# Kernel tuning notes

Measured on AMD Instinct MI355X. Metric: run time of the kernel, lower is better.

Reference implementation:

```python
import jax, jax.numpy as jnp
import numpy as np

B, L, D, H = 2, 4096, 1024, 4
DV = D // H
NP = 5
MIN_PROB = 0.01
CHUNK = 32
RIN = D + H * NP * 4 + H * (NP * (NP - 1)) // 2  # 1144
RH = 2 * RIN


def dwconv_causal(x, w):
    # x: (B, L, C); w: (C, K) depthwise causal FIR
    K = w.shape[-1]
    xp = jnp.pad(x, ((0, 0), (K - 1, 0), (0, 0))).transpose(0, 2, 1)  # (B,C,L+K-1)
    y = jax.lax.conv_general_dilated(
        xp, w[:, None, :], window_strides=(1,), padding='VALID',
        feature_group_count=w.shape[0],
        dimension_numbers=('NCH', 'OIH', 'NCH'))
    return y.transpose(0, 2, 1)  # (B,L,C)


def l2norm(x):
    return x * jax.lax.rsqrt(jnp.sum(x * x, -1, keepdims=True) + 1e-12)


def delta_rule_chunkwise(q, k, v, beta, chunk=CHUNK):
    # q,k: (b,h,L,dk)  v: (b,h,L,dv)  beta: (b,h,L); L divisible by chunk
    b, h, Lq, dk = q.shape
    dv = v.shape[-1]
    n = Lq // chunk
    q = l2norm(q); k = l2norm(k)
    v = v * beta[..., None]
    kb = k * beta[..., None]
    r = lambda x: x.reshape(b, h, n, chunk, -1)
    q, k, v, kb = r(q), r(k), r(v), r(kb)
    tri = jnp.triu(jnp.ones((chunk, chunk), bool), 0)
    attn = jnp.where(tri, 0.0, -(kb @ jnp.swapaxes(k, -1, -2)))
    for i in range(1, chunk):  # in-chunk triangular-inverse recurrence
        upd = jnp.einsum('...k,...ki->...i', attn[..., i, :], attn[..., :, :i])
        attn = attn.at[..., i, :i].add(upd)
    attn = attn + jnp.eye(chunk, dtype=attn.dtype)
    u = attn @ v
    w = attn @ kb
    strict = jnp.triu(jnp.ones((chunk, chunk), bool), 1)

    def step(S, inp):
        qi, ki, ui, wi = inp
        la = jnp.where(strict, 0.0, qi @ jnp.swapaxes(ki, -1, -2))
        u_i = ui - wi @ S
        o_i = qi @ S + la @ u_i
        return S + jnp.swapaxes(ki, -1, -2) @ u_i, o_i

    mv = lambda x: jnp.moveaxis(x, 2, 0)
    S0 = jnp.zeros((b, h, dk, dv), q.dtype)
    S, o = jax.lax.scan(step, S0, (mv(q), mv(k), mv(u), mv(w)))
    return jnp.moveaxis(o, 0, 2).reshape(b, h, Lq, dv), S


def setup_inputs() -> dict:
    key = jax.random.key(0)
    ks = jax.random.split(key, 20)
    f = lambda k, shape, s=0.02: jax.random.normal(k, shape, jnp.float32) * s
    # FIR filters: identity tap (last) + small noise, matching learned-from-delta init
    def fir(k, ksz):
        w = np.zeros((D, ksz), np.float32)
        w[:, -1] = 1.0
        return jnp.asarray(w) + f(k, (D, ksz), 0.02)
    b2 = np.zeros((H, NP), np.float32)
    b2[:, -1] = 0.5
    b2[:, -2] = 0.5
    return {
        'hidden_states': jax.random.normal(ks[0], (B, L, D), jnp.float32),
        'Wq': f(ks[1], (D, D)), 'Wk': f(ks[2], (D, D)), 'Wv': f(ks[3], (D, D)),
        'wq_conv': f(ks[4], (D, 4), 0.2), 'wk_conv': f(ks[5], (D, 4), 0.2),
        'wv_conv': f(ks[6], (D, 4), 0.2),
        'Wb': f(ks[7], (H, D)),
        'fir_s_w': fir(ks[8], 3), 'fir_m_w': fir(ks[9], 7),
        'fir_l_w': fir(ks[10], 25), 'fir_id_w': fir(ks[11], 1),
        'W1': f(ks[12], (RH, RIN)), 'b1': jnp.zeros((RH,), jnp.float32),
        'W2': f(ks[13], (H * NP, RH)), 'b2': jnp.asarray(b2.reshape(-1)),
        'norm_w': jnp.ones((DV,), jnp.float32),
        'Wo': f(ks[14], (D, D)),
    }


def reference(hidden_states, Wq, Wk, Wv, wq_conv, wk_conv, wv_conv, Wb,
              fir_s_w, fir_m_w, fir_l_w, fir_id_w, W1, b1, W2, b2, norm_w, Wo):
    silu = jax.nn.silu
    q = silu(dwconv_causal(hidden_states @ Wq.T, wq_conv))
    k = silu(dwconv_causal(hidden_states @ Wk.T, wk_conv))
    v = silu(dwconv_causal(hidden_states @ Wv.T, wv_conv))
    beta = jax.nn.sigmoid(hidden_states @ Wb.T)  # (B,L,H)
    q4 = q.reshape(B, L, H, -1).transpose(0, 2, 1, 3)
    k4 = k.reshape(B, L, H, -1).transpose(0, 2, 1, 3)
    v4 = v.reshape(B, L, H, -1).transpose(0, 2, 1, 3)
    delta_out, _ = delta_rule_chunkwise(q4, k4, v4, beta.transpose(0, 2, 1))
    delta_out = delta_out.transpose(0, 2, 1, 3)  # (B,L,H,DV)
    fir = lambda w: dwconv_causal(v, w).reshape(B, L, H, DV)
    branches = [fir(fir_s_w), fir(fir_m_w), fir(fir_l_w), delta_out, fir(fir_id_w)]
    feats = []
    for x in branches:
        sm = jax.nn.softmax(x, -1)
        feats += [x.mean(-1), jnp.var(x, -1, ddof=1), jnp.max(x, -1),
                  -(sm * jnp.log(sm + 1e-8)).sum(-1)]
    cross = []
    for i in range(NP):
        for j in range(i + 1, NP):
            xi, xj = branches[i], branches[j]
            den = jnp.sqrt(jnp.sum(xi * xi, -1)) * jnp.sqrt(jnp.sum(xj * xj, -1)) + 1e-8
            cross.append(jnp.sum(xi * xj, -1) / den)
    router_in = jnp.concatenate([hidden_states] + feats + cross, axis=-1)  # (B,L,RIN)
    hrt = jax.nn.gelu(router_in @ W1.T + b1, approximate=False)
    logits = (hrt @ W2.T + b2).reshape(B, L, H, NP)
    p = jax.nn.softmax(logits, -1)
    p = p * (1.0 - NP * MIN_PROB) + MIN_PROB  # probability floor
    out = jnp.einsum('blhp,pblhd->blhd', p, jnp.stack(branches))
    out = out * jax.lax.rsqrt(jnp.mean(out * out, -1, keepdims=True) + 1e-5) * norm_w
    return out.reshape(B, L, H * DV) @ Wo.T
```

## Files before the change

### kernel.cpp

```cpp
#include <hip/hip_runtime.h>
#include <stdint.h>

typedef unsigned short u16t;
typedef u16t us4 __attribute__((ext_vector_type(4)));
typedef u16t us8 __attribute__((ext_vector_type(8)));
typedef __bf16 bf8v __attribute__((ext_vector_type(8)));
typedef float f4 __attribute__((ext_vector_type(4)));

#define MFMA(a, b, c) __builtin_amdgcn_mfma_f32_16x16x32_bf16((a), (b), (c), 0, 0, 0)

__device__ __forceinline__ float bf2f(u16t u) {
  union { unsigned int i; float f; } c; c.i = ((unsigned int)u) << 16; return c.f;
}
__device__ __forceinline__ u16t f2bf(float f) {
  union { float f; unsigned int i; } c; c.f = f;
  return (u16t)((c.i + 0x7FFFu + ((c.i >> 16) & 1u)) >> 16);
}
__device__ __forceinline__ float wsum(float v) {
#pragma unroll
  for (int o = 32; o > 0; o >>= 1) v += __shfl_xor(v, o);
  return v;
}
__device__ __forceinline__ float wmax(float v) {
#pragma unroll
  for (int o = 32; o > 0; o >>= 1) v = fmaxf(v, __shfl_xor(v, o));
  return v;
}

template <bool AF32, bool BF32, bool CF32>
__global__ __launch_bounds__(256) void gemm_bt(const void* __restrict__ Av,
    const void* __restrict__ Btv, void* __restrict__ Cv,
    int M, int N, int K, int lda, int ldb, int ldc) {
  __shared__ u16t As[128][40];
  __shared__ u16t Bs[128][40];
  const int tid = threadIdx.x;
  const int m0 = blockIdx.y * 128, n0 = blockIdx.x * 128;
  const int wv = tid >> 6, l = tid & 63;
  const int wr = wv >> 1, wc = wv & 1;
  const int lr = l & 15, kg8 = (l >> 4) * 8, rg4 = (l >> 4) * 4;
  const int row_s = tid >> 1, seg = (tid & 1) * 16;
  const f4 zf = {0.f, 0.f, 0.f, 0.f};
  f4 acc[4][4];
#pragma unroll
  for (int i = 0; i < 4; ++i)
#pragma unroll
    for (int j = 0; j < 4; ++j) acc[i][j] = zf;

  for (int kt = 0; kt < K; kt += 32) {
    us8 a0, a1, b0, b1;
    if (AF32) {
      const float* pa = (const float*)Av + (size_t)(m0 + row_s) * lda + seg + kt;
      f4 fa0 = *(const f4*)(pa), fa1 = *(const f4*)(pa + 4);
      f4 fa2 = *(const f4*)(pa + 8), fa3 = *(const f4*)(pa + 12);
#pragma unroll
      for (int e = 0; e < 4; ++e) {
        a0[e] = f2bf(fa0[e]); a0[e + 4] = f2bf(fa1[e]);
        a1[e] = f2bf(fa2[e]); a1[e + 4] = f2bf(fa3[e]);
      }
    } else {
      const u16t* pa = (const u16t*)Av + (size_t)(m0 + row_s) * lda + seg + kt;
      a0 = *(const us8*)(pa); a1 = *(const us8*)(pa + 8);
    }
    if (BF32) {
      const float* pb = (const float*)Btv + (size_t)(n0 + row_s) * ldb + seg + kt;
      f4 fb0 = *(const f4*)(pb), fb1 = *(const f4*)(pb + 4);
      f4 fb2 = *(const f4*)(pb + 8), fb3 = *(const f4*)(pb + 12);
#pragma unroll
      for (int e = 0; e < 4; ++e) {
        b0[e] = f2bf(fb0[e]); b0[e + 4] = f2bf(fb1[e]);
        b1[e] = f2bf(fb2[e]); b1[e + 4] = f2bf(fb3[e]);
      }
    } else {
      const u16t* pb = (const u16t*)Btv + (size_t)(n0 + row_s) * ldb + seg + kt;
      b0 = *(const us8*)(pb); b1 = *(const us8*)(pb + 8);
    }
    *(us8*)&As[row_s][seg] = a0;
    *(us8*)&As[row_s][seg + 8] = a1;
    *(us8*)&Bs[row_s][seg] = b0;
    *(us8*)&Bs[row_s][seg + 8] = b1;
    __syncthreads();
    bf8v af[4], bg[4];
#pragma unroll
    for (int f = 0; f < 4; ++f) af[f] = *(const bf8v*)&As[wr * 64 + f * 16 + lr][kg8];
#pragma unroll
    for (int f = 0; f < 4; ++f) bg[f] = *(const bf8v*)&Bs[wc * 64 + f * 16 + lr][kg8];
#pragma unroll
    for (int i = 0; i < 4; ++i)
#pragma unroll
      for (int j = 0; j < 4; ++j) acc[i][j] = MFMA(af[i], bg[j], acc[i][j]);
    __syncthreads();
  }
#pragma unroll
  for (int i = 0; i < 4; ++i) {
    const int rb = m0 + wr * 64 + i * 16 + rg4;
#pragma unroll
    for (int j = 0; j < 4; ++j) {
      const int cb = n0 + wc * 64 + j * 16 + lr;
#pragma unroll
      for (int r = 0; r < 4; ++r) {
        if (CF32)
          ((float*)Cv)[(size_t)(rb + r) * ldc + cb] = acc[i][j][r];
        else
          ((u16t*)Cv)[(size_t)(rb + r) * ldc + cb] = f2bf(acc[i][j][r]);
      }
    }
  }
}

__global__ __launch_bounds__(256) void conv4_silu(
    const u16t* __restrict__ qlin, const u16t* __restrict__ klin, const u16t* __restrict__ vlin,
    const float* __restrict__ wq, const float* __restrict__ wk, const float* __restrict__ wvv,
    u16t* __restrict__ qc, u16t* __restrict__ kc, u16t* __restrict__ vc) {
  const int tid = threadIdx.x;
  const int l0 = blockIdx.x * 64;
  const int b = blockIdx.y >> 2, cb = blockIdx.y & 3;
  const int z = blockIdx.z;
  const u16t* in_ = (z == 0) ? qlin : ((z == 1) ? klin : vlin);
  const float* w_ = (z == 0) ? wq : ((z == 1) ? wk : wvv);
  u16t* out_ = (z == 0) ? qc : ((z == 1) ? kc : vc);
  const int c = cb * 256 + tid;
  __shared__ u16t sm[67][256];
  for (int i = 0; i < 67; ++i) {
    int ls = l0 - 3 + i;
    sm[i][tid] = (ls >= 0) ? in_[((size_t)b * 4096 + ls) * 1024 + c] : (u16t)0;
  }
  __syncthreads();
  f4 w4 = *(const f4*)&w_[c * 4];
  for (int ll = 0; ll < 64; ++ll) {
    float y = bf2f(sm[ll][tid]) * w4[0] + bf2f(sm[ll + 1][tid]) * w4[1] +
              bf2f(sm[ll + 2][tid]) * w4[2] + bf2f(sm[ll + 3][tid]) * w4[3];
    y = y / (1.f + expf(-y));
    out_[((size_t)b * 4096 + l0 + ll) * 1024 + c] = f2bf(y);
  }
}

__global__ __launch_bounds__(256) void beta_kernel(const float* __restrict__ hid,
    const float* __restrict__ Wb, float* __restrict__ beta) {
  const int m = blockIdx.x, tid = threadIdx.x;
  const int h = tid >> 6, l = tid & 63;
  float acc = 0.f;
#pragma unroll
  for (int it = 0; it < 4; ++it) {
    int kk = l * 4 + it * 256;
    f4 hv = *(const f4*)&hid[(size_t)m * 1024 + kk];
    f4 wv4 = *(const f4*)&Wb[(size_t)h * 1024 + kk];
#pragma unroll
    for (int e = 0; e < 4; ++e) acc += hv[e] * wv4[e];
  }
  acc = wsum(acc);
  if (l == 0) beta[m * 4 + h] = 1.f / (1.f + expf(-acc));
}

__global__ __launch_bounds__(256) void prep_kernel(u16t* __restrict__ qc, u16t* __restrict__ kc,
    const u16t* __restrict__ vc, const float* __restrict__ beta,
    u16t* __restrict__ kbeta, u16t* __restrict__ vbeta) {
  const int m = blockIdx.x, tid = threadIdx.x;
  const int h = tid >> 6, l = tid & 63;
  const size_t base = (size_t)m * 1024 + h * 256 + l * 4;
  const float bet = beta[m * 4 + h];
  us4 q4 = *(const us4*)&qc[base];
  float qf[4]; float ss = 0.f;
#pragma unroll
  for (int e = 0; e < 4; ++e) { qf[e] = bf2f(q4[e]); ss += qf[e] * qf[e]; }
  float qsc = rsqrtf(wsum(ss) + 1e-12f);
  us4 qo;
#pragma unroll
  for (int e = 0; e < 4; ++e) qo[e] = f2bf(qf[e] * qsc);
  *(us4*)&qc[base] = qo;
  us4 k4 = *(const us4*)&kc[base];
  float kf[4]; ss = 0.f;
#pragma unroll
  for (int e = 0; e < 4; ++e) { kf[e] = bf2f(k4[e]); ss += kf[e] * kf[e]; }
  float ksc = rsqrtf(wsum(ss) + 1e-12f);
  us4 ko, kbo;
#pragma unroll
  for (int e = 0; e < 4; ++e) {
    float kn = kf[e] * ksc;
    ko[e] = f2bf(kn);
    kbo[e] = f2bf(kn * bet);
  }
  *(us4*)&kc[base] = ko;
  *(us4*)&kbeta[base] = kbo;
  us4 v4 = *(const us4*)&vc[base];
  us4 vo;
#pragma unroll
  for (int e = 0; e < 4; ++e) vo[e] = f2bf(bf2f(v4[e]) * bet);
  *(us4*)&vbeta[base] = vo;
}

__global__ __launch_bounds__(256) void chunk_uw(const u16t* __restrict__ kn,
    const u16t* __restrict__ kbeta, const u16t* __restrict__ vbeta,
    u16t* __restrict__ ug, u16t* __restrict__ wg) {
  const int tid = threadIdx.x;
  const int bh = blockIdx.x >> 7, ci = blockIdx.x & 127;
  const int b = bh >> 2, h = bh & 3;
  const int l0 = ci * 32;
  __shared__ u16t kns[32][264], kbs[32][264], vbs[32][264];
  __shared__ float attn_s[32][33];
  const int sr = tid >> 5, sd8 = (tid & 31) * 8;
  const size_t rowbase = (size_t)b * 4096 * 1024 + (size_t)h * 256;
#pragma unroll
  for (int i = 0; i < 4; ++i) {
    int r = i * 8 + sr;
    size_t g = rowbase + (size_t)(l0 + r) * 1024 + sd8;
    *(us8*)&kns[r][sd8] = *(const us8*)&kn[g];
    *(us8*)&kbs[r][sd8] = *(const us8*)&kbeta[g];
    *(us8*)&vbs[r][sd8] = *(const us8*)&vbeta[g];
  }
  __syncthreads();
  {
    const int i = tid >> 3, j4 = (tid & 7) * 4;
    float d0 = 0.f, d1 = 0.f, d2 = 0.f, d3 = 0.f;
    for (int d8 = 0; d8 < 256; d8 += 8) {
      us8 kb8 = *(const us8*)&kbs[i][d8];
      us8 n0v = *(const us8*)&kns[j4][d8];
      us8 n1v = *(const us8*)&kns[j4 + 1][d8];
      us8 n2v = *(const us8*)&kns[j4 + 2][d8];
      us8 n3v = *(const us8*)&kns[j4 + 3][d8];
#pragma unroll
      for (int e = 0; e < 8; ++e) {
        float kv = bf2f(kb8[e]);
        d0 += kv * bf2f(n0v[e]); d1 += kv * bf2f(n1v[e]);
        d2 += kv * bf2f(n2v[e]); d3 += kv * bf2f(n3v[e]);
      }
    }
    attn_s[i][j4]     = (j4     < i) ? -d0 : 0.f;
    attn_s[i][j4 + 1] = (j4 + 1 < i) ? -d1 : 0.f;
    attn_s[i][j4 + 2] = (j4 + 2 < i) ? -d2 : 0.f;
    attn_s[i][j4 + 3] = (j4 + 3 < i) ? -d3 : 0.f;
  }
  __syncthreads();
  if (tid < 32) {
    const int j = tid;
    for (int i = 1; i < 32; ++i) {
      float aij = attn_s[i][j];
      float upd = 0.f;
#pragma unroll 1
      for (int k = 1; k < 31; ++k) {
        float aik = __shfl(aij, k);
        float akj = (k > j && k < i) ? attn_s[k][j] : 0.f;
        upd += aik * akj;
      }
      if (j < i) attn_s[i][j] = aij + upd;
    }
    attn_s[j][j] = 1.f;
  }
  __syncthreads();
  {
    const int r = tid >> 3, cg = (tid & 7) * 32;
    float ua[32], wa[32];
#pragma unroll
    for (int e = 0; e < 32; ++e) { ua[e] = 0.f; wa[e] = 0.f; }
    for (int j = 0; j < 32; ++j) {
      float a = attn_s[r][j];
#pragma unroll
      for (int e0 = 0; e0 < 32; e0 += 8) {
        us8 v8 = *(const us8*)&vbs[j][cg + e0];
        us8 k8 = *(const us8*)&kbs[j][cg + e0];
#pragma unroll
        for (int e = 0; e < 8; ++e) {
          ua[e0 + e] += a * bf2f(v8[e]);
          wa[e0 + e] += a * bf2f(k8[e]);
        }
      }
    }
    const size_t ob = ((size_t)bh * 4096 + l0 + r) * 256 + cg;
#pragma unroll
    for (int e0 = 0; e0 < 32; e0 += 8) {
      us8 pu, pw;
#pragma unroll
      for (int e = 0; e < 8; ++e) { pu[e] = f2bf(ua[e0 + e]); pw[e] = f2bf(wa[e0 + e]); }
      *(us8*)&ug[ob + e0] = pu;
      *(us8*)&wg[ob + e0] = pw;
    }
  }
}

__global__ __launch_bounds__(256, 1) void delta_scan(const u16t* __restrict__ qn,
    const u16t* __restrict__ kn, const u16t* __restrict__ ug, const u16t* __restrict__ wg,
    u16t* __restrict__ dout) {
  const int blk = blockIdx.x;
  const int bh = blk >> 2, vbidx = blk & 3;
  const int b = bh >> 2, h = bh & 3;
  const int c0 = vbidx * 64;
  const int tid = threadIdx.x;
  const int wv = tid >> 6, l = tid & 63;
  const int lr = l & 15, kg8 = (l >> 4) * 8, rg4 = (l >> 4) * 4;

  __shared__ u16t qs[32][264], ks2[32][264], wss[32][264];
  __shared__ u16t kts[256][40];
  __shared__ u16t sbf[64][264];
  __shared__ u16t las[32][40];
  __shared__ u16t uts[64][40];

  {
    u16t* sp = &sbf[0][0];
    for (int i = tid; i < 64 * 264; i += 256) sp[i] = 0;
  }
  const f4 zf = {0.f, 0.f, 0.f, 0.f};
  f4 sacc[16];
#pragma unroll
  for (int d = 0; d < 16; ++d) sacc[d] = zf;
  __syncthreads();

  const u16t* qb = qn + (size_t)b * 4096 * 1024 + (size_t)h * 256;
  const u16t* knb = kn + (size_t)b * 4096 * 1024 + (size_t)h * 256;
  const u16t* ub = ug + (size_t)bh * 4096 * 256;
  const u16t* wb = wg + (size_t)bh * 4096 * 256;
  const int sr = tid >> 5, sd8 = (tid & 31) * 8;

  us8 pq[4], pk[4], pw[4];
  us4 pu0, pu1;
  {
#pragma unroll
    for (int i = 0; i < 4; ++i) {
      const int r = i * 8 + sr;
      pq[i] = *(const us8*)(qb + (size_t)r * 1024 + sd8);
      pk[i] = *(const us8*)(knb + (size_t)r * 1024 + sd8);
      pw[i] = *(const us8*)(wb + (size_t)r * 256 + sd8);
    }
    pu0 = *(const us4*)(ub + (size_t)lr * 256 + c0 + wv * 16 + rg4);
    pu1 = *(const us4*)(ub + (size_t)(16 + lr) * 256 + c0 + wv * 16 + rg4);
  }

  for (int ci = 0; ci < 128; ++ci) {
    const int l0 = ci * 32;
#pragma unroll
    for (int i = 0; i < 4; ++i) {
      const int r = i * 8 + sr;
      *(us8*)&qs[r][sd8] = pq[i];
      *(us8*)&ks2[r][sd8] = pk[i];
      *(us8*)&wss[r][sd8] = pw[i];
    }
    const us4 u0 = pu0, u1 = pu1;
    __syncthreads();
    if (ci < 127) {
      const int l1 = l0 + 32;
#pragma unroll
      for (int i = 0; i < 4; ++i) {
        const int r = i * 8 + sr;
        pq[i] = *(const us8*)(qb + (size_t)(l1 + r) * 1024 + sd8);
        pk[i] = *(const us8*)(knb + (size_t)(l1 + r) * 1024 + sd8);
        pw[i] = *(const us8*)(wb + (size_t)(l1 + r) * 256 + sd8);
      }
      pu0 = *(const us4*)(ub + (size_t)(l1 + lr) * 256 + c0 + wv * 16 + rg4);
      pu1 = *(const us4*)(ub + (size_t)(l1 + 16 + lr) * 256 + c0 + wv * 16 + rg4);
    }
    {
      const int dk = tid;
      const int ps = ((dk >> 3) & 7) * 2;
#pragma unroll
      for (int w = 0; w < 16; ++w) {
        const int r = ((ps + w) & 15) * 2;
        unsigned int lo = ks2[r][dk], hi = ks2[r + 1][dk];
        *(unsigned int*)&kts[dk][r] = lo | (hi << 16);
      }
    }
    {
      const int rq = wv >> 1, rk = wv & 1;
      f4 t4 = zf;
#pragma unroll
      for (int ks = 0; ks < 8; ++ks) {
        bf8v a = *(const bf8v*)&qs[rq * 16 + lr][ks * 32 + kg8];
        bf8v bb = *(const bf8v*)&ks2[rk * 16 + lr][ks * 32 + kg8];
        t4 = MFMA(a, bb, t4);
      }
      const int colj = rk * 16 + lr;
#pragma unroll
      for (int rr = 0; rr < 4; ++rr) {
        const int rowr = rq * 16 + rg4 + rr;
        las[rowr][colj] = (colj <= rowr) ? f2bf(t4[rr]) : (u16t)0;
      }
    }
    {
      f4 m0 = zf, m1 = zf;
#pragma unroll
      for (int ks = 0; ks < 8; ++ks) {
        bf8v a = *(const bf8v*)&sbf[wv * 16 + lr][ks * 32 + kg8];
        bf8v bb0 = *(const bf8v*)&wss[lr][ks * 32 + kg8];
        bf8v bb1 = *(const bf8v*)&wss[16 + lr][ks * 32 + kg8];
        m0 = MFMA(a, bb0, m0);
        m1 = MFMA(a, bb1, m1);
      }
#pragma unroll
      for (int rt = 0; rt < 2; ++rt) {
        f4 mm = rt ? m1 : m0;
        const us4 uu = rt ? u1 : u0;
        const int r = rt * 16 + lr;
#pragma unroll
        for (int rr = 0; rr < 4; ++rr)
          uts[wv * 16 + rg4 + rr][r] = f2bf(bf2f(uu[rr]) - mm[rr]);
      }
    }
    __syncthreads();
    {
      f4 o0 = zf, o1 = zf;
#pragma unroll
      for (int ks = 0; ks < 8; ++ks) {
        bf8v a = *(const bf8v*)&sbf[wv * 16 + lr][ks * 32 + kg8];
        bf8v bb0 = *(const bf8v*)&qs[lr][ks * 32 + kg8];
        bf8v bb1 = *(const bf8v*)&qs[16 + lr][ks * 32 + kg8];
        o0 = MFMA(a, bb0, o0);
        o1 = MFMA(a, bb1, o1);
      }
      bf8v a2 = *(const bf8v*)&uts[wv * 16 + lr][kg8];
      {
        bf8v lb0 = *(const bf8v*)&las[lr][kg8];
        bf8v lb1 = *(const bf8v*)&las[16 + lr][kg8];
        o0 = MFMA(a2, lb0, o0);
        o1 = MFMA(a2, lb1, o1);
      }
#pragma unroll
      for (int rt = 0; rt < 2; ++rt) {
        f4 oo = rt ? o1 : o0;
        const int r = rt * 16 + lr;
        us4 st;
#pragma unroll
        for (int rr = 0; rr < 4; ++rr) st[rr] = f2bf(oo[rr]);
        *(us4*)(dout + ((size_t)(b * 4096 + l0 + r) * 4 + h) * 256 + c0 + wv * 16 + rg4) = st;
      }
#pragma unroll
      for (int d = 0; d < 16; ++d) {
        bf8v bb = *(const bf8v*)&kts[d * 16 + lr][kg8];
        sacc[d] = MFMA(a2, bb, sacc[d]);
      }
#pragma unroll
      for (int d = 0; d < 16; ++d) {
#pragma unroll
        for (int rr = 0; rr < 4; ++rr)
          sbf[wv * 16 + rg4 + rr][d * 16 + lr] = f2bf(sacc[d][rr]);
      }
    }
    __syncthreads();
  }
}

__global__ __launch_bounds__(256) void fir_kernel(const u16t* __restrict__ vc,
    const float* __restrict__ w3g, const float* __restrict__ w7g,
    const float* __restrict__ w25g, const float* __restrict__ w1g,
    u16t* __restrict__ fs, u16t* __restrict__ fm, u16t* __restrict__ fl,
    u16t* __restrict__ fid) {
  const int tid = threadIdx.x;
  const int l0 = blockIdx.x * 64;
  const int b = blockIdx.y >> 2, cb = blockIdx.y & 3;
  const int c = cb * 256 + tid;
  __shared__ u16t sm[88][256];
  for (int i = 0; i < 88; ++i) {
    int ls = l0 - 24 + i;
    sm[i][tid] = (ls >= 0) ? vc[((size_t)b * 4096 + ls) * 1024 + c] : (u16t)0;
  }
  __syncthreads();
  float w3[3], w7[7], w25[25], w1_;
#pragma unroll
  for (int j = 0; j < 3; ++j) w3[j] = w3g[c * 3 + j];
#pragma unroll
  for (int j = 0; j < 7; ++j) w7[j] = w7g[c * 7 + j];
#pragma unroll
  for (int j = 0; j < 25; ++j) w25[j] = w25g[c * 25 + j];
  w1_ = w1g[c];
  for (int ll = 0; ll < 64; ++ll) {
    float x[25];
#pragma unroll
    for (int j = 0; j < 25; ++j) x[j] = bf2f(sm[ll + j][tid]);
    float ys = x[22] * w3[0] + x[23] * w3[1] + x[24] * w3[2];
    float ym = 0.f;
#pragma unroll
    for (int j = 0; j < 7; ++j) ym += x[18 + j] * w7[j];
    float yl = 0.f;
#pragma unroll
    for (int j = 0; j < 25; ++j) yl += x[j] * w25[j];
    float yi = x[24] * w1_;
    const size_t o = ((size_t)b * 4096 + l0 + ll) * 1024 + c;
    fs[o] = f2bf(ys); fm[o] = f2bf(ym); fl[o] = f2bf(yl); fid[o] = f2bf(yi);
  }
}

__global__ __launch_bounds__(256) void features_kernel(const float* __restrict__ hid,
    const u16t* __restrict__ p0, const u16t* __restrict__ p1, const u16t* __restrict__ p2,
    const u16t* __restrict__ p3, const u16t* __restrict__ p4, u16t* __restrict__ router) {
  const int m = blockIdx.x, tid = threadIdx.x;
  const int h = tid >> 6, l = tid & 63;
  const size_t base = (size_t)m * 1024 + h * 256 + l * 4;
  const u16t* bp[5] = {p0, p1, p2, p3, p4};
  float x[5][4];
#pragma unroll
  for (int br = 0; br < 5; ++br) {
    us4 v = *(const us4*)&bp[br][base];
#pragma unroll
    for (int e = 0; e < 4; ++e) x[br][e] = bf2f(v[e]);
  }
  float s1[5], s2[5], mx[5];
#pragma unroll
  for (int br = 0; br < 5; ++br) {
    float a = 0.f, bq = 0.f, m_ = -1e30f;
#pragma unroll
    for (int e = 0; e < 4; ++e) {
      a += x[br][e]; bq += x[br][e] * x[br][e]; m_ = fmaxf(m_, x[br][e]);
    }
    s1[br] = wsum(a); s2[br] = wsum(bq); mx[br] = wmax(m_);
  }
  float ent[5];
#pragma unroll
  for (int br = 0; br < 5; ++br) {
    float e_ = 0.f;
#pragma unroll
    for (int e = 0; e < 4; ++e) e_ += expf(x[br][e] - mx[br]);
    float es = wsum(e_);
    float hn = 0.f;
#pragma unroll
    for (int e = 0; e < 4; ++e) {
      float pv = expf(x[br][e] - mx[br]) / es;
      hn += pv * logf(pv + 1e-8f);
    }
    ent[br] = -wsum(hn);
  }
  float dt[10];
  {
    int pi = 0;
#pragma unroll
    for (int i = 0; i < 5; ++i)
#pragma unroll
      for (int j = i + 1; j < 5; ++j) {
        float d = 0.f;
#pragma unroll
        for (int e = 0; e < 4; ++e) d += x[i][e] * x[j][e];
        dt[pi] = wsum(d);
        ++pi;
      }
  }
  if (l == 0) {
    u16t* rp = router + (size_t)m * 1152 + 1024;
#pragma unroll
    for (int br = 0; br < 5; ++br) {
      float mean = s1[br] * (1.f / 256.f);
      float var = (s2[br] - s1[br] * s1[br] * (1.f / 256.f)) * (1.f / 255.f);
      rp[br * 16 + 0 + h] = f2bf(mean);
      rp[br * 16 + 4 + h] = f2bf(var);
      rp[br * 16 + 8 + h] = f2bf(mx[br]);
      rp[br * 16 + 12 + h] = f2bf(ent[br]);
    }
    int pi = 0;
#pragma unroll
    for (int i = 0; i < 5; ++i)
#pragma unroll
      for (int j = i + 1; j < 5; ++j) {
        float den = sqrtf(s2[i]) * sqrtf(s2[j]) + 1e-8f;
        rp[80 + pi * 4 + h] = f2bf(dt[pi] / den);
        ++pi;
      }
  }
  {
    f4 hv = *(const f4*)&hid[(size_t)m * 1024 + tid * 4];
    us4 hv4;
#pragma unroll
    for (int e = 0; e < 4; ++e) hv4[e] = f2bf(hv[e]);
    *(us4*)&router[(size_t)m * 1152 + tid * 4] = hv4;
  }
  if (tid < 8) router[(size_t)m * 1152 + 1144 + tid] = 0;
}

__global__ __launch_bounds__(256) void gelu_bias(u16t* __restrict__ hrt,
    const float* __restrict__ b1) {
  const size_t idx = ((size_t)blockIdx.x * 256 + threadIdx.x) * 4;
  const int col = (int)(idx % 2304);
  us4 v = *(const us4*)&hrt[idx];
  us4 o;
#pragma unroll
  for (int e = 0; e < 4; ++e) {
    int cc = col + e;
    float xx = bf2f(v[e]) + ((cc < 2288) ? b1[cc] : 0.f);
    float g = 0.5f * xx * (1.f + erff(xx * 0.70710678118f));
    o[e] = f2bf(g);
  }
  *(us4*)&hrt[idx] = o;
}

__global__ __launch_bounds__(256) void w2_softmax(const u16t* __restrict__ hrt,
    const float* __restrict__ W2, const float* __restrict__ b2, float* __restrict__ pout) {
  const int m = blockIdx.x, tid = threadIdx.x;
  const int h = tid >> 6, l = tid & 63;
  float acc[5];
#pragma unroll
  for (int n = 0; n < 5; ++n) acc[n] = 0.f;
  for (int kk = l * 4; kk < 2288; kk += 256) {
    us4 hv = *(const us4*)&hrt[(size_t)m * 2304 + kk];
    float hf[4];
#pragma unroll
    for (int e = 0; e < 4; ++e) hf[e] = bf2f(hv[e]);
#pragma unroll
    for (int n = 0; n < 5; ++n) {
      f4 wv4 = *(const f4*)&W2[(size_t)(h * 5 + n) * 2288 + kk];
#pragma unroll
      for (int e = 0; e < 4; ++e) acc[n] += hf[e] * wv4[e];
    }
  }
#pragma unroll
  for (int n = 0; n < 5; ++n) acc[n] = wsum(acc[n]);
  if (l == 0) {
    float lg[5];
#pragma unroll
    for (int n = 0; n < 5; ++n) lg[n] = acc[n] + b2[h * 5 + n];
    float mxv = lg[0];
#pragma unroll
    for (int n = 1; n < 5; ++n) mxv = fmaxf(mxv, lg[n]);
    float es = 0.f, ev[5];
#pragma unroll
    for (int n = 0; n < 5; ++n) { ev[n] = expf(lg[n] - mxv); es += ev[n]; }
#pragma unroll
    for (int n = 0; n < 5; ++n)
      pout[(size_t)m * 20 + h * 5 + n] = (ev[n] / es) * 0.95f + 0.01f;
  }
}

__global__ __launch_bounds__(256) void mix_kernel(const u16t* __restrict__ p0,
    const u16t* __restrict__ p1, const u16t* __restrict__ p2, const u16t* __restrict__ p3,
    const u16t* __restrict__ p4, const float* __restrict__ pbuf,
    const float* __restrict__ normw, u16t* __restrict__ mixed) {
  const int m = blockIdx.x, tid = threadIdx.x;
  const int h = tid >> 6, l = tid & 63;
  const size_t base = (size_t)m * 1024 + h * 256 + l * 4;
  const u16t* bp[5] = {p0, p1, p2, p3, p4};
  float p5[5];
#pragma unroll
  for (int n = 0; n < 5; ++n) p5[n] = pbuf[(size_t)m * 20 + h * 5 + n];
  float o[4] = {0.f, 0.f, 0.f, 0.f};
#pragma unroll
  for (int br = 0; br < 5; ++br) {
    us4 v = *(const us4*)&bp[br][base];
#pragma unroll
    for (int e = 0; e < 4; ++e) o[e] += p5[br] * bf2f(v[e]);
  }
  float ss = 0.f;
#pragma unroll
  for (int e = 0; e < 4; ++e) ss += o[e] * o[e];
  ss = wsum(ss);
  float sc = rsqrtf(ss * (1.f / 256.f) + 1e-5f);
  f4 nw = *(const f4*)&normw[l * 4];
  us4 ov;
#pragma unroll
  for (int e = 0; e < 4; ++e) ov[e] = f2bf(o[e] * sc * nw[e]);
  *(us4*)&mixed[base] = ov;
}

__global__ __launch_bounds__(256) void pad_w1(const float* __restrict__ W1,
    u16t* __restrict__ W1p) {
  size_t idx = (size_t)blockIdx.x * 256 + threadIdx.x;
  if (idx >= (size_t)2304 * 1152) return;
  int n = (int)(idx / 1152), k = (int)(idx % 1152);
  W1p[idx] = (n < 2288 && k < 1144) ? f2bf(W1[(size_t)n * 1144 + k]) : (u16t)0;
}

extern "C" void kernel_launch(void* const* d_in, const int* in_sizes, int n_in,
                              void* d_out, int out_size, void* d_ws, size_t ws_size,
                              hipStream_t stream) {
  (void)in_sizes; (void)n_in; (void)out_size; (void)ws_size;
  const float* hid = (const float*)d_in[0];
  const float* Wq = (const float*)d_in[1];
  const float* Wk = (const float*)d_in[2];
  const float* Wv = (const float*)d_in[3];
  const float* wqc = (const float*)d_in[4];
  const float* wkc = (const float*)d_in[5];
  const float* wvc = (const float*)d_in[6];
  const float* Wb = (const float*)d_in[7];
  const float* fsw = (const float*)d_in[8];
  const float* fmw = (const float*)d_in[9];
  const float* flw = (const float*)d_in[10];
  const float* fiw = (const float*)d_in[11];
  const float* W1 = (const float*)d_in[12];
  const float* b1 = (const float*)d_in[13];
  const float* W2 = (const float*)d_in[14];
  const float* b2 = (const float*)d_in[15];
  const float* nwt = (const float*)d_in[16];
  const float* Wo = (const float*)d_in[17];
  float* out = (float*)d_out;

  char* wsp = (char*)d_ws;
  const size_t S = (size_t)2 * 4096 * 1024 * 2;
  u16t* ql = (u16t*)(wsp + 0 * S);
  u16t* kl = (u16t*)(wsp + 1 * S);
  u16t* vl = (u16t*)(wsp + 2 * S);
  u16t* qc = (u16t*)(wsp + 3 * S);
  u16t* kc = (u16t*)(wsp + 4 * S);
  u16t* vc = (u16t*)(wsp + 5 * S);
  u16t* ubuf = (u16t*)(wsp + 6 * S);
  u16t* wbuf = (u16t*)(wsp + 7 * S);
  char* p = wsp + 8 * S;
  u16t* router = (u16t*)p; p += (size_t)8192 * 1152 * 2;
  u16t* hrt = (u16t*)p;    p += (size_t)8192 * 2304 * 2;
  u16t* w1p = (u16t*)p;    p += (size_t)2304 * 1152 * 2;
  float* pbuf = (float*)p; p += (size_t)8192 * 20 * 4;
  float* beta = (float*)p; p += (size_t)8192 * 4 * 4;
  u16t* kbeta = ql;
  u16t* vbeta = kl;
  u16t* dlt = kl;
  u16t* f_s = vl;
  u16t* f_m = qc;
  u16t* f_l = kc;
  u16t* f_i = ubuf;
  u16t* mixed = wbuf;

  dim3 blk(256);
  gemm_bt<true, true, false><<<dim3(8, 64), blk, 0, stream>>>(hid, Wq, ql, 8192, 1024, 1024, 1024, 1024, 1024);
  gemm_bt<true, true, false><<<dim3(8, 64), blk, 0, stream>>>(hid, Wk, kl, 8192, 1024, 1024, 1024, 1024, 1024);
  gemm_bt<true, true, false><<<dim3(8, 64), blk, 0, stream>>>(hid, Wv, vl, 8192, 1024, 1024, 1024, 1024, 1024);
  conv4_silu<<<dim3(64, 8, 3), blk, 0, stream>>>(ql, kl, vl, wqc, wkc, wvc, qc, kc, vc);
  beta_kernel<<<dim3(8192), blk, 0, stream>>>(hid, Wb, beta);
  prep_kernel<<<dim3(8192), blk, 0, stream>>>(qc, kc, vc, beta, kbeta, vbeta);
  chunk_uw<<<dim3(1024), blk, 0, stream>>>(kc, kbeta, vbeta, ubuf, wbuf);
  delta_scan<<<dim3(32), blk, 0, stream>>>(qc, kc, ubuf, wbuf, dlt);
  fir_kernel<<<dim3(64, 8), blk, 0, stream>>>(vc, fsw, fmw, flw, fiw, f_s, f_m, f_l, f_i);
  features_kernel<<<dim3(8192), blk, 0, stream>>>(hid, f_s, f_m, f_l, dlt, f_i, router);
  pad_w1<<<dim3(10368), blk, 0, stream>>>(W1, w1p);
  gemm_bt<false, false, false><<<dim3(18, 64), blk, 0, stream>>>(router, w1p, hrt, 8192, 2304, 1152, 1152, 1152, 2304);
  gelu_bias<<<dim3(18432), blk, 0, stream>>>(hrt, b1);
  w2_softmax<<<dim3(8192), blk, 0, stream>>>(hrt, W2, b2, pbuf);
  mix_kernel<<<dim3(8192), blk, 0, stream>>>(f_s, f_m, f_l, dlt, f_i, pbuf, nwt, mixed);
  gemm_bt<false, true, true><<<dim3(8, 64), blk, 0, stream>>>(mixed, Wo, out, 8192, 1024, 1024, 1024, 1024, 1024);
}
```

Before: 1.151 ms.

## Batch QKV GEMMs into one launch and restructure delta scan LDS access

The three Q/K/V projection GEMMs are merged into a single launch that picks its weight and output by blockIdx.z, giving the GPU one larger grid and fewer launches. In the delta scan kernel, the k-transpose store into LDS now uses an XOR swizzle with a matching swizzled read, replacing the rotated write order, to reduce bank conflicts. The q·S MFMAs are moved before the barrier and interleaved with the w·S MFMAs, since both read the same S fragment. The risks are the correctness of the swizzle index math and higher register pressure in the scan kernel.

Result: no change. 1.136 ms (-1.2%).

```diff
diff --git a/kernel.cpp b/kernel.cpp
--- a/kernel.cpp
+++ b/kernel.cpp
@@ -28,13 +28,12 @@
 }
 
 template <bool AF32, bool BF32, bool CF32>
-__global__ __launch_bounds__(256) void gemm_bt(const void* __restrict__ Av,
+__device__ __forceinline__ void gemm_body(const void* __restrict__ Av,
     const void* __restrict__ Btv, void* __restrict__ Cv,
-    int M, int N, int K, int lda, int ldb, int ldc) {
+    int K, int lda, int ldb, int ldc, int m0, int n0) {
   __shared__ u16t As[128][40];
   __shared__ u16t Bs[128][40];
   const int tid = threadIdx.x;
-  const int m0 = blockIdx.y * 128, n0 = blockIdx.x * 128;
   const int wv = tid >> 6, l = tid & 63;
   const int wr = wv >> 1, wc = wv & 1;
   const int lr = l & 15, kg8 = (l >> 4) * 8, rg4 = (l >> 4) * 4;
@@ -105,6 +104,25 @@
       }
     }
   }
+}
+
+template <bool AF32, bool BF32, bool CF32>
+__global__ __launch_bounds__(256) void gemm_bt(const void* __restrict__ Av,
+    const void* __restrict__ Btv, void* __restrict__ Cv,
+    int K, int lda, int ldb, int ldc) {
+  gemm_body<AF32, BF32, CF32>(Av, Btv, Cv, K, lda, ldb, ldc,
+                              blockIdx.y * 128, blockIdx.x * 128);
+}
+
+__global__ __launch_bounds__(256) void gemm_qkv3(const float* __restrict__ A,
+    const float* __restrict__ B0, const float* __restrict__ B1,
+    const float* __restrict__ B2, u16t* __restrict__ C0, u16t* __restrict__ C1,
+    u16t* __restrict__ C2v) {
+  const int z = blockIdx.z;
+  const float* Bt = (z == 0) ? B0 : ((z == 1) ? B1 : B2);
+  u16t* C = (z == 0) ? C0 : ((z == 1) ? C1 : C2v);
+  gemm_body<true, true, false>(A, Bt, C, 1024, 1024, 1024, 1024,
+                               blockIdx.y * 128, blockIdx.x * 128);
 }
 
 __global__ __launch_bounds__(256) void conv4_silu(
@@ -348,12 +366,11 @@
     }
     {
       const int dk = tid;
-      const int ps = ((dk >> 3) & 7) * 2;
-#pragma unroll
-      for (int w = 0; w < 16; ++w) {
-        const int r = ((ps + w) & 15) * 2;
+      const int swz = ((dk >> 3) & 3) << 3;
+#pragma unroll
+      for (int r = 0; r < 32; r += 2) {
         unsigned int lo = ks2[r][dk], hi = ks2[r + 1][dk];
-        *(unsigned int*)&kts[dk][r] = lo | (hi << 16);
+        *(unsigned int*)&kts[dk][r ^ swz] = lo | (hi << 16);
       }
     }
     {
@@ -372,15 +389,20 @@
         las[rowr][colj] = (colj <= rowr) ? f2bf(t4[rr]) : (u16t)0;
       }
     }
+    f4 o0 = zf, o1 = zf;
     {
       f4 m0 = zf, m1 = zf;
 #pragma unroll
       for (int ks = 0; ks < 8; ++ks) {
         bf8v a = *(const bf8v*)&sbf[wv * 16 + lr][ks * 32 + kg8];
-        bf8v bb0 = *(const bf8v*)&wss[lr][ks * 32 + kg8];
-        bf8v bb1 = *(const bf8v*)&wss[16 + lr][ks * 32 + kg8];
-        m0 = MFMA(a, bb0, m0);
-        m1 = MFMA(a, bb1, m1);
+        bf8v wb0 = *(const bf8v*)&wss[lr][ks * 32 + kg8];
+        bf8v wb1 = *(const bf8v*)&wss[16 + lr][ks * 32 + kg8];
+        bf8v qb0 = *(const bf8v*)&qs[lr][ks * 32 + kg8];
+        bf8v qb1 = *(const bf8v*)&qs[16 + lr][ks * 32 + kg8];
+        m0 = MFMA(a, wb0, m0);
+        m1 = MFMA(a, wb1, m1);
+        o0 = MFMA(a, qb0, o0);
+        o1 = MFMA(a, qb1, o1);
       }
 #pragma unroll
       for (int rt = 0; rt < 2; ++rt) {
@@ -394,15 +416,6 @@
     }
     __syncthreads();
     {
-      f4 o0 = zf, o1 = zf;
-#pragma unroll
-      for (int ks = 0; ks < 8; ++ks) {
-        bf8v a = *(const bf8v*)&sbf[wv * 16 + lr][ks * 32 + kg8];
-        bf8v bb0 = *(const bf8v*)&qs[lr][ks * 32 + kg8];
-        bf8v bb1 = *(const bf8v*)&qs[16 + lr][ks * 32 + kg8];
-        o0 = MFMA(a, bb0, o0);
-        o1 = MFMA(a, bb1, o1);
-      }
       bf8v a2 = *(const bf8v*)&uts[wv * 16 + lr][kg8];
       {
         bf8v lb0 = *(const bf8v*)&las[lr][kg8];
@@ -421,7 +434,8 @@
       }
 #pragma unroll
       for (int d = 0; d < 16; ++d) {
-        bf8v bb = *(const bf8v*)&kts[d * 16 + lr][kg8];
+        const int swzd = ((2 * d + (lr >> 3)) & 3) << 3;
+        bf8v bb = *(const bf8v*)&kts[d * 16 + lr][kg8 ^ swzd];
         sacc[d] = MFMA(a2, bb, sacc[d]);
       }
 #pragma unroll
@@ -700,9 +714,7 @@
   u16t* mixed = wbuf;
 
   dim3 blk(256);
-  gemm_bt<true, true, false><<<dim3(8, 64), blk, 0, stream>>>(hid, Wq, ql, 8192, 1024, 1024, 1024, 1024, 1024);
-  gemm_bt<true, true, false><<<dim3(8, 64), blk, 0, stream>>>(hid, Wk, kl, 8192, 1024, 1024, 1024, 1024, 1024);
-  gemm_bt<true, true, false><<<dim3(8, 64), blk, 0, stream>>>(hid, Wv, vl, 8192, 1024, 1024, 1024, 1024, 1024);
+  gemm_qkv3<<<dim3(8, 64, 3), blk, 0, stream>>>(hid, Wq, Wk, Wv, ql, kl, vl);
   conv4_silu<<<dim3(64, 8, 3), blk, 0, stream>>>(ql, kl, vl, wqc, wkc, wvc, qc, kc, vc);
   beta_kernel<<<dim3(8192), blk, 0, stream>>>(hid, Wb, beta);
   prep_kernel<<<dim3(8192), blk, 0, stream>>>(qc, kc, vc, beta, kbeta, vbeta);
@@ -711,9 +723,9 @@
   fir_kernel<<<dim3(64, 8), blk, 0, stream>>>(vc, fsw, fmw, flw, fiw, f_s, f_m, f_l, f_i);
   features_kernel<<<dim3(8192), blk, 0, stream>>>(hid, f_s, f_m, f_l, dlt, f_i, router);
   pad_w1<<<dim3(10368), blk, 0, stream>>>(W1, w1p);
-  gemm_bt<false, false, false><<<dim3(18, 64), blk, 0, stream>>>(router, w1p, hrt, 8192, 2304, 1152, 1152, 1152, 2304);
+  gemm_bt<false, false, false><<<dim3(18, 64), blk, 0, stream>>>(router, w1p, hrt, 1152, 1152, 1152, 2304);
   gelu_bias<<<dim3(18432), blk, 0, stream>>>(hrt, b1);
   w2_softmax<<<dim3(8192), blk, 0, stream>>>(hrt, W2, b2, pbuf);
   mix_kernel<<<dim3(8192), blk, 0, stream>>>(f_s, f_m, f_l, dlt, f_i, pbuf, nwt, mixed);
-  gemm_bt<false, true, true><<<dim3(8, 64), blk, 0, stream>>>(mixed, Wo, out, 8192, 1024, 1024, 1024, 1024, 1024);
-}
+  gemm_bt<false, true, true><<<dim3(8, 64), blk, 0, stream>>>(mixed, Wo, out, 1024, 1024, 1024, 1024);
+}
```
